# Kernel optimization log

Measured on AMD Instinct MI355X. Metric: run time of the kernel, lower is better.

Reference implementation:

```python
import jax, jax.numpy as jnp
import numpy as np

NUM_GROUPS = 8
INPUT_DIM = 1024
OUTPUT_DIM = 1024
TOKENS_PER_GROUP = 8192  # rows per group after reshape


def setup_inputs() -> dict:
    key = jax.random.key(0)
    kx, kw = jax.random.split(key)
    # x: [N*G, D_in] as fed to the torch module (it reshapes internally)
    x = jax.random.normal(kx, (TOKENS_PER_GROUP * NUM_GROUPS, INPUT_DIM), dtype=jnp.float32)
    # Stacked per-group Linear weights, torch layout [D_out, D_in] per group.
    # Xavier-normal gain=1: std = sqrt(2 / (fan_in + fan_out))
    std = np.sqrt(2.0 / (INPUT_DIM + OUTPUT_DIM)).astype(np.float32)
    W = jax.random.normal(kw, (NUM_GROUPS, OUTPUT_DIM, INPUT_DIM), dtype=jnp.float32) * std
    return {"x": x, "W": W}


def reference(x, W):
    # x: [N*G, D_in] -> [N, G, D_in]
    n = x.shape[0] // NUM_GROUPS
    xg = x.reshape(n, NUM_GROUPS, INPUT_DIM)
    # per-group linear: out[n,g,k] = sum_d xg[n,g,d] * W[g,k,d]
    out = jnp.einsum("ngd,gkd->ngk", xg, W)
    return out.reshape(-1, OUTPUT_DIM)
```

## Files before the change

### kernel.cpp

```cpp
#include <hip/hip_runtime.h>
#include <hip/hip_bf16.h>


namespace {

constexpr int NG   = 8;
constexpr int DIN  = 1024;
constexpr int DOUT = 1024;
constexpr int BM   = 256;
constexpr int BN   = 256;
constexpr int BK   = 64;
constexpr int NKT  = DIN / BK;
constexpr int ROWB = BK * 2;
constexpr int TILE = BM * ROWB;
constexpr int LDS_BYTES = 4 * TILE;
constexpr int JTN  = DOUT / BN;
constexpr size_t WSB_BYTES = (size_t)NG * JTN * NKT * TILE;

typedef __attribute__((ext_vector_type(8))) short bf16x8;
typedef __attribute__((ext_vector_type(4))) float f32x4;

__device__ __forceinline__ bf16x8 pack_bf16x8v(f32x4 lo, f32x4 hi) {
  union { __hip_bfloat162 h2[4]; bf16x8 v; } p;
  p.h2[0] = __float22bfloat162_rn(make_float2(lo.x, lo.y));
  p.h2[1] = __float22bfloat162_rn(make_float2(lo.z, lo.w));
  p.h2[2] = __float22bfloat162_rn(make_float2(hi.x, hi.y));
  p.h2[3] = __float22bfloat162_rn(make_float2(hi.z, hi.w));
  return p.v;
}

__device__ __forceinline__ void glds16(const void* g, void* l) {
  __builtin_amdgcn_global_load_lds(
      (const __attribute__((address_space(1))) unsigned int*)g,
      (__attribute__((address_space(3))) unsigned int*)l, 16, 0, 0);
}

#define FENCE() asm volatile("" ::: "memory")
#define BAR()   do { FENCE(); __builtin_amdgcn_s_barrier(); FENCE(); } while (0)
#define LGKM0() asm volatile("s_waitcnt lgkmcnt(0)" ::: "memory")
#define VM0()   asm volatile("s_waitcnt vmcnt(0)" ::: "memory")
#define VMC8()  asm volatile("s_waitcnt vmcnt(8)" ::: "memory")
#define MFMA_(a, b, c) __builtin_amdgcn_mfma_f32_16x16x32_bf16((a), (b), (c), 0, 0, 0)

__global__ __launch_bounds__(256)
void cvt_w_kernel(const float* __restrict__ W, char* __restrict__ wsB) {
  const int q    = (int)blockIdx.x * 256 + (int)threadIdx.x;
  const int tile = q >> 13;
  const int q13  = q & 8191;
  const int r    = q13 >> 5;
  const int cp   = q13 & 31;
  const int g    = tile >> 6;
  const int jt   = (tile >> 4) & 3;
  const int kt   = tile & 15;

  const float2 s = *(const float2*)(
      W + ((size_t)(g * DOUT + jt * BN + r)) * DIN + kt * 64 + 2 * cp);
  union { __hip_bfloat162 h; unsigned u; } pk;
  pk.h = __float22bfloat162_rn(make_float2(s.x, s.y));

  const int swzr = (r & 7) << 4;
  const int dstByte = r * ROWB + (((cp >> 2) * 16) ^ swzr) + (cp & 3) * 4;
  *(unsigned*)(wsB + (size_t)tile * TILE + dstByte) = pk.u;
}

#define STAGE_T(T, dA, dB)                                                     \
  {                                                                            \
    const float* Ai = aSrc + (size_t)(T) * BK;                                 \
    _Pragma("unroll")                                                          \
    for (int p = 0; p < 8; ++p) {                                              \
      aL[2 * p]     = *(const f32x4*)(Ai + p * ARSTR);                         \
      aL[2 * p + 1] = *(const f32x4*)(Ai + p * ARSTR + 4);                     \
    }                                                                          \
    FENCE();                                                                   \
    if (WSB) {                                                                 \
      const char* Bi = BgT + (size_t)(T) * TILE;                               \
      _Pragma("unroll")                                                        \
      for (int p = 0; p < 8; ++p)                                              \
        glds16(Bi + dst0 + p * 4096, (dB) + dst0 + p * 4096);                  \
    } else {                                                                   \
      const float* Bi = bSrc + (size_t)(T) * BK;                               \
      _Pragma("unroll")                                                        \
      for (int p = 0; p < 8; ++p) {                                            \
        bL[2 * p]     = *(const f32x4*)(Bi + p * BRSTR);                       \
        bL[2 * p + 1] = *(const f32x4*)(Bi + p * BRSTR + 4);                   \
      }                                                                        \
    }                                                                          \
    FENCE();                                                                   \
    if (WSB) { VMC8(); } else { VM0(); }                                       \
    _Pragma("unroll")                                                          \
    for (int p = 0; p < 8; ++p)                                                \
      *(bf16x8*)((dA) + dst0 + p * 4096) =                                     \
          pack_bf16x8v(aL[2 * p], aL[2 * p + 1]);                              \
    if (!WSB) {                                                                \
      _Pragma("unroll")                                                        \
      for (int p = 0; p < 8; ++p)                                              \
        *(bf16x8*)((dB) + dst0 + p * 4096) =                                   \
            pack_bf16x8v(bL[2 * p], bL[2 * p + 1]);                            \
    }                                                                          \
    if (WSB) { VM0(); }                                                        \
    LGKM0();                                                                   \
  }

template <bool WSB>
__global__ __launch_bounds__(768, 3)
void gemm_ws(const float* __restrict__ X, const float* __restrict__ W,
             const char* __restrict__ wsB, float* __restrict__ O) {
  extern __shared__ char smem[];
  char* const smA = smem;
  char* const smB = smem + 2 * TILE;

  const int bid = (int)blockIdx.x;
  const int swz = (bid & 7) * 128 + (bid >> 3);
  const int jt = swz & 3;
  const int it = (swz >> 2) & 31;
  const int g  = swz >> 7;

  const int n0 = it * BM;
  const int c0 = jt * BN;

  const int tid  = (int)threadIdx.x;
  const int lane = tid & 63;
  const int wid  = tid >> 6;

  if (wid < 8) {
    const int wr = (wid >> 2) & 1;
    const int wc = wid & 3;
    const int fr = lane & 15;
    const int fq = lane >> 4;
    const int colx0 = ((fq       ^ (fr & 7)) << 4);
    const int colx1 = (((4 + fq) ^ (fr & 7)) << 4);
    const int aRow0 = (wr * 128 + fr) * ROWB;
    const int bRow0 = (wc * 64  + fr) * ROWB;

    f32x4 acc[8][4];
#pragma unroll
    for (int m = 0; m < 8; ++m)
#pragma unroll
      for (int n = 0; n < 4; ++n) acc[m][n] = (f32x4){0.f, 0.f, 0.f, 0.f};

    BAR();

    for (int t = 0; t < NKT; ++t) {
      char* const cA = smA + (t & 1) * TILE;
      char* const cB = smB + (t & 1) * TILE;
#pragma unroll
      for (int ks = 0; ks < 2; ++ks) {
        const int cx = ks ? colx1 : colx0;
        bf16x8 bfr[4];
#pragma unroll
        for (int n = 0; n < 4; ++n)
          bfr[n] = *(const bf16x8*)(cB + bRow0 + n * 2048 + cx);
        __builtin_amdgcn_s_setprio(1);
#pragma unroll
        for (int m = 0; m < 8; ++m) {
          bf16x8 am = *(const bf16x8*)(cA + aRow0 + m * 2048 + cx);
#pragma unroll
          for (int n = 0; n < 4; ++n)
            acc[m][n] = MFMA_(am, bfr[n], acc[m][n]);
        }
        __builtin_amdgcn_s_setprio(0);
      }
      if (t + 1 < NKT) BAR();
    }

#pragma unroll
    for (int m = 0; m < 8; ++m) {
#pragma unroll
      for (int r = 0; r < 4; ++r) {
        const int row = wr * 128 + m * 16 + fq * 4 + r;
        float* orow = O + ((size_t)(n0 + row) * NG + g) * DOUT + c0 + wc * 64;
#pragma unroll
        for (int n = 0; n < 4; ++n) {
          orow[n * 16 + fr] = acc[m][n][r];
        }
      }
    }
  } else {
    const int ptid = tid - 512;
    const int r0   = ptid >> 3;
    const int sl   = ptid & 7;
    const int lg   = sl ^ (r0 & 7);
    const int dst0 = ptid * 16;

    const float* aSrc = X + ((size_t)(n0 + r0) * NG + g) * DIN + lg * 8;
    constexpr size_t ARSTR = (size_t)32 * NG * DIN;
    const char* BgT = wsB + (size_t)((g * JTN + jt) * NKT) * TILE;
    const float* bSrc = W + ((size_t)(g * DOUT + c0 + r0)) * DIN + lg * 8;
    constexpr size_t BRSTR = (size_t)32 * DIN;

    f32x4 aL[16];
    f32x4 bL[16];

    STAGE_T(0, smA, smB);
    BAR();

    for (int t = 0; t + 1 < NKT; ++t) {
      char* const nA = smA + ((t + 1) & 1) * TILE;
      char* const nB = smB + ((t + 1) & 1) * TILE;
      STAGE_T(t + 1, nA, nB);
      BAR();
    }
  }
}

}

extern "C" void kernel_launch(void* const* d_in, const int* in_sizes, int n_in,
                              void* d_out, int out_size, void* d_ws, size_t ws_size,
                              hipStream_t stream) {
  (void)n_in; (void)out_size;
  const float* X = (const float*)d_in[0];
  const float* W = (const float*)d_in[1];
  float* O = (float*)d_out;

  const int tokens_total = in_sizes[0] / DIN;
  const int ntok_per_g   = tokens_total / NG;
  const int grid = NG * (ntok_per_g / BM) * (DOUT / BN);

  if (ws_size >= WSB_BYTES) {
    const int cvt_grid = (int)(WSB_BYTES / 4 / 256);
    cvt_w_kernel<<<dim3(cvt_grid), dim3(256), 0, stream>>>(W, (char*)d_ws);
    (void)hipFuncSetAttribute((const void*)gemm_ws<true>,
                              hipFuncAttributeMaxDynamicSharedMemorySize,
                              LDS_BYTES);
    gemm_ws<true><<<dim3(grid), dim3(768), LDS_BYTES, stream>>>(
        X, W, (const char*)d_ws, O);
  } else {
    (void)hipFuncSetAttribute((const void*)gemm_ws<false>,
                              hipFuncAttributeMaxDynamicSharedMemorySize,
                              LDS_BYTES);
    gemm_ws<false><<<dim3(grid), dim3(768), LDS_BYTES, stream>>>(
        X, W, nullptr, O);
  }
}
```

Baseline: 217.9 us.

## Prefetch X tiles two stages ahead in producer warps with register double-buffering

```diff
diff --git a/kernel.cpp b/kernel.cpp
--- a/kernel.cpp
+++ b/kernel.cpp
@@ -39,7 +39,7 @@
 #define BAR()   do { FENCE(); __builtin_amdgcn_s_barrier(); FENCE(); } while (0)
 #define LGKM0() asm volatile("s_waitcnt lgkmcnt(0)" ::: "memory")
 #define VM0()   asm volatile("s_waitcnt vmcnt(0)" ::: "memory")
-#define VMC8()  asm volatile("s_waitcnt vmcnt(8)" ::: "memory")
+#define VMC16() asm volatile("s_waitcnt vmcnt(16)" ::: "memory")
 #define MFMA_(a, b, c) __builtin_amdgcn_mfma_f32_16x16x32_bf16((a), (b), (c), 0, 0, 0)
 
 __global__ __launch_bounds__(256)
@@ -63,42 +63,35 @@
   *(unsigned*)(wsB + (size_t)tile * TILE + dstByte) = pk.u;
 }
 
-#define STAGE_T(T, dA, dB)                                                     \
-  {                                                                            \
-    const float* Ai = aSrc + (size_t)(T) * BK;                                 \
+#define ISSUE_A(TT, CUR)                                                       \
+  { const float* Ai = aSrc + (size_t)(TT) * BK;                                \
     _Pragma("unroll")                                                          \
     for (int p = 0; p < 8; ++p) {                                              \
-      aL[2 * p]     = *(const f32x4*)(Ai + p * ARSTR);                         \
-      aL[2 * p + 1] = *(const f32x4*)(Ai + p * ARSTR + 4);                     \
-    }                                                                          \
+      aL[CUR][2 * p]     = *(const f32x4*)(Ai + p * ARSTR);                    \
+      aL[CUR][2 * p + 1] = *(const f32x4*)(Ai + p * ARSTR + 4);                \
+    } }
+
+#define WRITE_A(CUR, DBUF)                                                     \
+  { _Pragma("unroll")                                                          \
+    for (int p = 0; p < 8; ++p)                                                \
+      *(bf16x8*)((DBUF) + dst0 + p * 4096) =                                   \
+          pack_bf16x8v(aL[CUR][2 * p], aL[CUR][2 * p + 1]); }
+
+#define PBODY(T, CUR)                                                          \
+  {                                                                            \
+    char* const nA = smA + (((T) + 1) & 1) * TILE;                             \
+    char* const nB = smB + (((T) + 1) & 1) * TILE;                             \
+    const char* Bi = BgT + (size_t)((T) + 1) * TILE;                           \
+    _Pragma("unroll")                                                          \
+    for (int p = 0; p < 8; ++p)                     \
+      glds16(Bi + dst0 + p * 4096, nB + dst0 + p * 4096);                      \
     FENCE();                                                                   \
-    if (WSB) {                                                                 \
-      const char* Bi = BgT + (size_t)(T) * TILE;                               \
-      _Pragma("unroll")                                                        \
-      for (int p = 0; p < 8; ++p)                                              \
-        glds16(Bi + dst0 + p * 4096, (dB) + dst0 + p * 4096);                  \
-    } else {                                                                   \
-      const float* Bi = bSrc + (size_t)(T) * BK;                               \
-      _Pragma("unroll")                                                        \
-      for (int p = 0; p < 8; ++p) {                                            \
-        bL[2 * p]     = *(const f32x4*)(Bi + p * BRSTR);                       \
-        bL[2 * p + 1] = *(const f32x4*)(Bi + p * BRSTR + 4);                   \
-      }                                                                        \
-    }                                                                          \
+    if ((T) + 2 < NKT) ISSUE_A((T) + 2, CUR);                                  \
     FENCE();                                                                   \
-    if (WSB) { VMC8(); } else { VM0(); }                                       \
-    _Pragma("unroll")                                                          \
-    for (int p = 0; p < 8; ++p)                                                \
-      *(bf16x8*)((dA) + dst0 + p * 4096) =                                     \
-          pack_bf16x8v(aL[2 * p], aL[2 * p + 1]);                              \
-    if (!WSB) {                                                                \
-      _Pragma("unroll")                                                        \
-      for (int p = 0; p < 8; ++p)                                              \
-        *(bf16x8*)((dB) + dst0 + p * 4096) =                                   \
-            pack_bf16x8v(bL[2 * p], bL[2 * p + 1]);                            \
-    }                                                                          \
-    if (WSB) { VM0(); }                                                        \
+    WRITE_A((CUR) ^ 1, nA);                    \
     LGKM0();                                                                   \
+    if ((T) + 2 < NKT) { VMC16(); } else { VM0(); }                            \
+    BAR();                                                                     \
   }
 
 template <bool WSB>
@@ -188,17 +181,60 @@
     const float* bSrc = W + ((size_t)(g * DOUT + c0 + r0)) * DIN + lg * 8;
     constexpr size_t BRSTR = (size_t)32 * DIN;
 
-    f32x4 aL[16];
-    f32x4 bL[16];
-
-    STAGE_T(0, smA, smB);
-    BAR();
-
-    for (int t = 0; t + 1 < NKT; ++t) {
-      char* const nA = smA + ((t + 1) & 1) * TILE;
-      char* const nB = smB + ((t + 1) & 1) * TILE;
-      STAGE_T(t + 1, nA, nB);
+    f32x4 aL[2][16];
+
+    if (WSB) {
+#pragma unroll
+      for (int p = 0; p < 8; ++p)
+        glds16(BgT + dst0 + p * 4096, smB + dst0 + p * 4096);
+      FENCE();
+      ISSUE_A(0, 0);
+      ISSUE_A(1, 1);
+      FENCE();
+      WRITE_A(0, smA);
+      LGKM0();
       BAR();
+
+      for (int tt = 0; tt + 1 < NKT; tt += 2) {
+        PBODY(tt, 0);
+        if (tt + 2 < NKT) PBODY(tt + 1, 1);
+      }
+    } else {
+      f32x4 bL[16];
+#pragma unroll
+      for (int p = 0; p < 8; ++p) {
+        aL[0][2 * p]     = *(const f32x4*)(aSrc + p * ARSTR);
+        aL[0][2 * p + 1] = *(const f32x4*)(aSrc + p * ARSTR + 4);
+        bL[2 * p]        = *(const f32x4*)(bSrc + p * BRSTR);
+        bL[2 * p + 1]    = *(const f32x4*)(bSrc + p * BRSTR + 4);
+      }
+      WRITE_A(0, smA);
+#pragma unroll
+      for (int p = 0; p < 8; ++p)
+        *(bf16x8*)(smB + dst0 + p * 4096) =
+            pack_bf16x8v(bL[2 * p], bL[2 * p + 1]);
+      LGKM0();
+      BAR();
+      for (int t = 0; t + 1 < NKT; ++t) {
+        char* const nA = smA + ((t + 1) & 1) * TILE;
+        char* const nB = smB + ((t + 1) & 1) * TILE;
+        const float* Ai = aSrc + (size_t)(t + 1) * BK;
+        const float* Bi = bSrc + (size_t)(t + 1) * BK;
+#pragma unroll
+        for (int p = 0; p < 8; ++p) {
+          aL[0][2 * p]     = *(const f32x4*)(Ai + p * ARSTR);
+          aL[0][2 * p + 1] = *(const f32x4*)(Ai + p * ARSTR + 4);
+          bL[2 * p]        = *(const f32x4*)(Bi + p * BRSTR);
+          bL[2 * p + 1]    = *(const f32x4*)(Bi + p * BRSTR + 4);
+        }
+        WRITE_A(0, nA);
+#pragma unroll
+        for (int p = 0; p < 8; ++p)
+          *(bf16x8*)(nB + dst0 + p * 4096) =
+              pack_bf16x8v(bL[2 * p], bL[2 * p + 1]);
+        LGKM0();
+        BAR();
+      }
     }
   }
 }
```

Result: faster. 213.2 us (median of 13 runs) (-2.2%).
